# Kernel tuning notes

Hardware: AMD Instinct MI355X
Metric: run time of the kernel (lower is better)

## Reference

```python
import jax, jax.numpy as jnp
import numpy as np

N_NODES = 100000
N_EDGES = 1600000
N_CRYS = 2000
NODE_F = 64
EDGE_F = 41
N_CONV = 3
H_F = 128
EPS = 1e-5


def _seg_mean(v, idx, n):
    s = jax.ops.segment_sum(v, idx, num_segments=n)
    c = jax.ops.segment_sum(jnp.ones((v.shape[0], 1), v.dtype), idx, num_segments=n)
    return s / jnp.maximum(c, 1.0)


def _bn(x, g, b):
    # training-mode batch norm over dim 0, biased variance (torch semantics)
    m = x.mean(axis=0)
    v = x.var(axis=0)
    return (x - m) * jax.lax.rsqrt(v + EPS) * g + b


def setup_inputs() -> dict:
    key = jax.random.key(0)
    ks = jax.random.split(key, 16)
    inp = {}
    inp['node_fea'] = jax.random.randint(ks[0], (N_NODES,), 0, 101)
    inp['edge_fea'] = jax.random.normal(ks[1], (N_EDGES, EDGE_F), dtype=jnp.float32)
    inp['idx1'] = jax.random.randint(ks[2], (N_EDGES,), 0, N_NODES)
    inp['idx2'] = jax.random.randint(ks[3], (N_EDGES,), 0, N_NODES)
    inp['idx3'] = jnp.sort(jax.random.randint(ks[4], (N_NODES,), 0, N_CRYS))
    # parameters
    din = 2 * NODE_F + EDGE_F
    sc = 1.0 / np.sqrt(din)
    inp['emb'] = jax.random.normal(ks[5], (101, NODE_F), dtype=jnp.float32)
    inp['Wf'] = jax.random.uniform(ks[6], (N_CONV, din, 2 * NODE_F), jnp.float32, -sc, sc)
    inp['bf'] = jax.random.uniform(ks[7], (N_CONV, 2 * NODE_F), jnp.float32, -sc, sc)
    inp['g1'] = jnp.ones((N_CONV, 2 * NODE_F), jnp.float32)
    inp['be1'] = jnp.zeros((N_CONV, 2 * NODE_F), jnp.float32)
    inp['g2'] = jnp.ones((N_CONV, NODE_F), jnp.float32)
    inp['be2'] = jnp.zeros((N_CONV, NODE_F), jnp.float32)
    sc2 = 1.0 / np.sqrt(NODE_F)
    inp['Wc'] = jax.random.uniform(ks[8], (NODE_F, H_F), jnp.float32, -sc2, sc2)
    inp['bc'] = jax.random.uniform(ks[9], (H_F,), jnp.float32, -sc2, sc2)
    sc3 = 1.0 / np.sqrt(H_F)
    inp['Wo'] = jax.random.uniform(ks[10], (H_F, 2), jnp.float32, -sc3, sc3)
    inp['bo'] = jax.random.uniform(ks[11], (2,), jnp.float32, -sc3, sc3)
    return inp


def reference(node_fea, edge_fea, idx1, idx2, idx3, emb, Wf, bf, g1, be1, g2, be2, Wc, bc, Wo, bo):
    x = emb[node_fea]                                   # [N, 64]
    for l in range(N_CONV):
        z12 = jnp.concatenate([x[idx1], x[idx2], edge_fea], axis=1)   # [E, 169]
        z12 = _bn(z12 @ Wf[l] + bf[l], g1[l], be1[l])   # [E, 128]
        gate, conv = jnp.split(z12, 2, axis=1)
        msg = jax.nn.sigmoid(gate) * jax.nn.softplus(conv)
        node_new = _bn(_seg_mean(msg, idx1, N_NODES), g2[l], be2[l])
        x = jax.nn.softplus(x + node_new)
    crys = _seg_mean(x, idx3, N_CRYS)                   # [C, 64]
    crys = jax.nn.softplus(crys @ Wc + bc)              # [C, 128]
    return crys @ Wo + bo                               # [C, 2]
```

## Files before the change

### kernel.cpp

```cpp
#include <hip/hip_runtime.h>
#include <hip/hip_bf16.h>


#define NN 100000
#define NE 1600000
#define NC 2000
#define KPAD 176
#define NFRAG 11
#define EFW 48
#define EPSB 1e-5f
#define NCH 1000
#define CH 100

typedef _Float16 f16;
typedef _Float16 half8 __attribute__((ext_vector_type(8)));
typedef _Float16 half2v __attribute__((ext_vector_type(2)));
typedef float f32x16 __attribute__((ext_vector_type(16)));

__device__ __forceinline__ f32x16 zero16() {
    f32x16 v;
#pragma unroll
    for (int i = 0; i < 16; i++) v[i] = 0.f;
    return v;
}
__device__ __forceinline__ float fsoftplus(float x) {
    return fmaxf(x, 0.f) + __logf(1.f + __expf(-fabsf(x)));
}
__device__ __forceinline__ float fsigmoid(float x) {
    return __fdividef(1.f, 1.f + __expf(-x));
}

__global__ void k_prep_x(const int* __restrict__ nf, const float* __restrict__ emb,
                         float* __restrict__ xf, f16* __restrict__ x16) {
    for (int idx = blockIdx.x * blockDim.x + threadIdx.x; idx < NN * 64;
         idx += gridDim.x * blockDim.x) {
        int n = idx >> 6, k = idx & 63;
        float v = emb[nf[n] * 64 + k];
        xf[idx] = v;
        x16[idx] = (f16)v;
    }
}

__global__ void k_deg(const int* __restrict__ idx1, const int* __restrict__ idx3,
                      int* deg1, float* cnt3) {
    for (int i = blockIdx.x * blockDim.x + threadIdx.x; i < NE;
         i += gridDim.x * blockDim.x) {
        atomicAdd(&deg1[idx1[i]], 1);
        if (i < NN) atomicAdd(&cnt3[idx3[i]], 1.f);
    }
}

__global__ void k_scan_a(const int* __restrict__ deg, int* __restrict__ csum) {
    int t = blockIdx.x * blockDim.x + threadIdx.x;
    if (t < NCH) {
        int s = 0;
        int base = t * CH;
        for (int i = 0; i < CH; i++) s += deg[base + i];
        csum[t] = s;
    }
}
__global__ void k_scan_b(const int* __restrict__ csum, int* __restrict__ coff) {
    __shared__ int sc[256];
    int t = threadIdx.x;
    int v[4];
    int part = 0;
#pragma unroll
    for (int q = 0; q < 4; q++) {
        int idx = 4 * t + q;
        v[q] = (idx < NCH) ? csum[idx] : 0;
        part += v[q];
    }
    sc[t] = part;
    __syncthreads();
    for (int off = 1; off < 256; off <<= 1) {
        int add = (t >= off) ? sc[t - off] : 0;
        __syncthreads();
        sc[t] += add;
        __syncthreads();
    }
    int run = sc[t] - part;
#pragma unroll
    for (int q = 0; q < 4; q++) {
        int idx = 4 * t + q;
        if (idx < NCH) coff[idx] = run;
        run += v[q];
    }
}
__global__ void k_scan_c(const int* __restrict__ deg, const int* __restrict__ coff,
                         int* __restrict__ rp) {
    int t = blockIdx.x * blockDim.x + threadIdx.x;
    if (t < NCH) {
        int running = coff[t];
        int base = t * CH;
        for (int i = 0; i < CH; i++) {
            rp[base + i] = running;
            running += deg[base + i];
        }
    }
}

__global__ void k_scatter(const int* __restrict__ idx1, const int* __restrict__ idx2,
                          const int* __restrict__ rp1, int* cur1, int* elist1,
                          int* i1r, int* i2r) {
    for (int e = blockIdx.x * blockDim.x + threadIdx.x; e < NE;
         e += gridDim.x * blockDim.x) {
        int n1 = idx1[e];
        int p = rp1[n1] + atomicAdd(&cur1[n1], 1);
        elist1[p] = e;
        i1r[p] = n1;
        i2r[p] = idx2[e];
    }
}

__global__ void k_prep_efg(const float* __restrict__ ef, const int* __restrict__ elist1,
                           f16* __restrict__ ef16p) {
    for (long idx = (long)blockIdx.x * blockDim.x + threadIdx.x; idx < (long)NE * EFW;
         idx += (long)gridDim.x * blockDim.x) {
        long p = idx / EFW;
        int k = (int)(idx - p * EFW);
        int e = elist1[p];
        float v = (k < 41) ? ef[(size_t)e * 41 + k] : 0.f;
        ef16p[idx] = (f16)v;
    }
}

__global__ void k_wt(const float* __restrict__ Wf_l, f16* __restrict__ WTp) {
    for (int idx = blockIdx.x * blockDim.x + threadIdx.x; idx < 128 * KPAD;
         idx += gridDim.x * blockDim.x) {
        int sl = idx / KPAD, k = idx % KPAD;
        int g = sl >> 5, cl = sl & 31;
        int col = (cl & 16) ? 64 + g * 16 + (cl & 15) : g * 16 + cl;
        float v = (k < 169) ? Wf_l[k * 128 + col] : 0.f;
        WTp[idx] = (f16)v;
    }
}

__global__ __launch_bounds__(256) void k_edge_a(
    const f16* __restrict__ x16, const f16* __restrict__ ef16p,
    const f16* __restrict__ WTp, const int* __restrict__ i1r,
    const int* __restrict__ i2r, float* __restrict__ estats,
    f16* __restrict__ zph) {
    __shared__ f16 ldsB[NFRAG][128][16];
    __shared__ float lst[256];
    int tid = threadIdx.x;
    for (int i = tid; i < NFRAG * 128 * 2; i += 256) {
        int s = i >> 8, rem = i & 255;
        int slot = rem >> 1, half = rem & 1;
        *reinterpret_cast<half8*>(&ldsB[s][slot][half * 8]) =
            *reinterpret_cast<const half8*>(WTp + slot * KPAD + s * 16 + half * 8);
    }
    lst[tid] = 0.f;
    __syncthreads();

    int lane = tid & 63;
    int c = lane & 31, kg = lane >> 5;
    const int zbase = 2 * (c & 15) + ((c >> 4) & 1);
    const int ldso = c * 32 + kg * 16;

    float s1[4] = {0.f, 0.f, 0.f, 0.f}, s2[4] = {0.f, 0.f, 0.f, 0.f};

    const int NT = NE / 32;
    const int wstride = gridDim.x * 4;
    int t = blockIdx.x * 4 + (tid >> 6);

    half8 a[NFRAG];
    {
        size_t pb = (size_t)t * 32 + c;
        int i1v = i1r[pb], i2v = i2r[pb];
#pragma unroll
        for (int s = 0; s < 4; s++)
            a[s] = *reinterpret_cast<const half8*>(x16 + (size_t)i1v * 64 + s * 16 + kg * 8);
#pragma unroll
        for (int s = 0; s < 4; s++)
            a[4 + s] = *reinterpret_cast<const half8*>(x16 + (size_t)i2v * 64 + s * 16 + kg * 8);
#pragma unroll
        for (int s = 0; s < 3; s++)
            a[8 + s] = __builtin_nontemporal_load(
                reinterpret_cast<const half8*>(ef16p + pb * EFW + s * 16 + kg * 8));
    }
    int tn = t + wstride;
    int i1n = 0, i2n = 0;
    if (tn < NT) {
        i1n = i1r[(size_t)tn * 32 + c];
        i2n = i2r[(size_t)tn * 32 + c];
    }

    while (true) {
        bool hasn = (tn < NT);
        half8 nx[NFRAG];
        int i1nn = 0, i2nn = 0;
        if (hasn) {
#pragma unroll
            for (int s = 0; s < 4; s++)
                nx[s] = *reinterpret_cast<const half8*>(x16 + (size_t)i1n * 64 + s * 16 + kg * 8);
#pragma unroll
            for (int s = 0; s < 4; s++)
                nx[4 + s] = *reinterpret_cast<const half8*>(x16 + (size_t)i2n * 64 + s * 16 + kg * 8);
#pragma unroll
            for (int s = 0; s < 3; s++)
                nx[8 + s] = __builtin_nontemporal_load(reinterpret_cast<const half8*>(
                    ef16p + ((size_t)tn * 32 + c) * EFW + s * 16 + kg * 8));
            int tnn = tn + wstride;
            if (tnn < NT) {
                i1nn = i1r[(size_t)tnn * 32 + c];
                i2nn = i2r[(size_t)tnn * 32 + c];
            }
        }
        int p0 = t * 32;
#pragma unroll
        for (int g = 0; g < 4; g++) {
            f32x16 acc = zero16();
#pragma unroll
            for (int s = 0; s < NFRAG; s++) {
                half8 b = *reinterpret_cast<const half8*>(
                    reinterpret_cast<const char*>(&ldsB[0][0][0]) + s * 4096 + g * 1024 + ldso);
                acc = __builtin_amdgcn_mfma_f32_32x32x16_f16(a[s], b, acc, 0, 0, 0);
            }
#pragma unroll
            for (int r = 0; r < 16; r++) {
                float v = acc[r];
                s1[g] += v;
                s2[g] += v * v;
                int row = (r & 3) + 8 * (r >> 2) + 4 * kg;
                __builtin_nontemporal_store(
                    (f16)v, zph + (size_t)(p0 + row) * 128 + 32 * g + zbase);
            }
        }
        if (!hasn) break;
        t = tn;
        tn += wstride;
#pragma unroll
        for (int s = 0; s < NFRAG; s++) a[s] = nx[s];
        i1n = i1nn;
        i2n = i2nn;
    }
#pragma unroll
    for (int g = 0; g < 4; g++) {
        s1[g] += __shfl_xor(s1[g], 32, 64);
        s2[g] += __shfl_xor(s2[g], 32, 64);
    }
    if (kg == 0) {
#pragma unroll
        for (int g = 0; g < 4; g++) {
            int jz = (c & 16) ? 64 + g * 16 + (c & 15) : g * 16 + c;
            atomicAdd(&lst[jz], s1[g]);
            atomicAdd(&lst[128 + jz], s2[g]);
        }
    }
    __syncthreads();
    atomicAdd(&estats[tid], lst[tid]);
}

__global__ __launch_bounds__(256) void k_nodered(
    const half2v* __restrict__ zp, const int* __restrict__ rp1,
    const int* __restrict__ deg1, const float* __restrict__ estats,
    const float* __restrict__ g1, const float* __restrict__ be1,
    float* __restrict__ raw_out, float* __restrict__ nstats) {
    __shared__ float sstat[128];
    int tid = threadIdx.x;
    int j = tid & 63, wv = tid >> 6;
    if (tid < 128) sstat[tid] = 0.f;
    __syncthreads();
    float mg = estats[j] * (1.f / NE);
    float vg = estats[128 + j] * (1.f / NE) - mg * mg;
    float ag = g1[j] * rsqrtf(vg + EPSB);
    float bg = be1[j] - mg * ag;
    float mc = estats[64 + j] * (1.f / NE);
    float vc = estats[192 + j] * (1.f / NE) - mc * mc;
    float ac = g1[64 + j] * rsqrtf(vc + EPSB);
    float bc = be1[64 + j] - mc * ac;
    float p1 = 0.f, p2 = 0.f;
    for (int n = blockIdx.x * 4 + wv; n < NN; n += gridDim.x * 4) {
        int st = rp1[n], d = deg1[n];
        float acc = 0.f;
#pragma unroll 4
        for (int q = 0; q < d; q++) {
            half2v z = __builtin_nontemporal_load(&zp[(size_t)(st + q) * 64 + j]);
            float g = fsigmoid((float)z[0] * ag + bg);
            float s = fsoftplus((float)z[1] * ac + bc);
            acc += g * s;
        }
        float raw = acc / fmaxf((float)d, 1.f);
        raw_out[(size_t)n * 64 + j] = raw;
        p1 += raw;
        p2 += raw * raw;
    }
    atomicAdd(&sstat[j], p1);
    atomicAdd(&sstat[64 + j], p2);
    __syncthreads();
    if (tid < 128) atomicAdd(&nstats[tid], sstat[tid]);
}

template <bool LAST>
__global__ __launch_bounds__(256) void k_node_apply(
    const float* __restrict__ raw_in, const float* __restrict__ nstats,
    const float* __restrict__ g2, const float* __restrict__ be2,
    float* __restrict__ xf, f16* __restrict__ x16, const int* __restrict__ idx3,
    float* __restrict__ crsum) {
    for (int idx = blockIdx.x * blockDim.x + threadIdx.x; idx < NN * 64;
         idx += gridDim.x * blockDim.x) {
        int n = idx >> 6, j = idx & 63;
        float m = nstats[j] * (1.f / NN);
        float var = nstats[64 + j] * (1.f / NN) - m * m;
        float rs = rsqrtf(var + EPSB);
        float a = g2[j] * rs;
        float b = be2[j] - m * a;
        float v = fsoftplus(xf[idx] + raw_in[idx] * a + b);
        if (LAST) {
            atomicAdd(&crsum[(size_t)idx3[n] * 64 + j], v);
        } else {
            xf[idx] = v;
            x16[idx] = (f16)v;
        }
    }
}

__global__ __launch_bounds__(128) void k_out(const float* __restrict__ crsum,
                                             const float* __restrict__ cnt3,
                                             const float* __restrict__ Wc,
                                             const float* __restrict__ bcv,
                                             const float* __restrict__ Wo,
                                             const float* __restrict__ bo,
                                             float* __restrict__ out) {
    __shared__ float crym[64];
    __shared__ float red[4];
    int c = blockIdx.x, tid = threadIdx.x;
    if (tid < 64) crym[tid] = crsum[c * 64 + tid] / fmaxf(cnt3[c], 1.f);
    __syncthreads();
    float hv = bcv[tid];
#pragma unroll
    for (int k = 0; k < 64; k++) hv += crym[k] * Wc[k * 128 + tid];
    hv = fsoftplus(hv);
    float o0 = hv * Wo[tid * 2 + 0];
    float o1 = hv * Wo[tid * 2 + 1];
#pragma unroll
    for (int off = 32; off > 0; off >>= 1) {
        o0 += __shfl_down(o0, off, 64);
        o1 += __shfl_down(o1, off, 64);
    }
    int wv = tid >> 6;
    if ((tid & 63) == 0) { red[wv * 2] = o0; red[wv * 2 + 1] = o1; }
    __syncthreads();
    if (tid == 0) {
        out[c * 2 + 0] = red[0] + red[2] + bo[0];
        out[c * 2 + 1] = red[1] + red[3] + bo[1];
    }
}

static inline size_t al256(size_t x) { return (x + 255) & ~(size_t)255; }

extern "C" void kernel_launch(void* const* d_in, const int* in_sizes, int n_in,
                              void* d_out, int out_size, void* d_ws, size_t ws_size,
                              hipStream_t stream) {
    const int* node_fea = (const int*)d_in[0];
    const float* edge_fea = (const float*)d_in[1];
    const int* idx1 = (const int*)d_in[2];
    const int* idx2 = (const int*)d_in[3];
    const int* idx3 = (const int*)d_in[4];
    const float* emb = (const float*)d_in[5];
    const float* Wf = (const float*)d_in[6];
    const float* g1 = (const float*)d_in[8];
    const float* be1 = (const float*)d_in[9];
    const float* g2 = (const float*)d_in[10];
    const float* be2 = (const float*)d_in[11];
    const float* Wc = (const float*)d_in[12];
    const float* bc = (const float*)d_in[13];
    const float* Wo = (const float*)d_in[14];
    const float* bo = (const float*)d_in[15];
    float* out = (float*)d_out;
    unsigned char* ws = (unsigned char*)d_ws;

    size_t off = 0;
    size_t o_xf = off;     off = al256(off + (size_t)NN * 64 * 4);
    size_t o_x16 = off;    off = al256(off + (size_t)NN * 64 * 2);
    size_t o_efp = off;    off = al256(off + (size_t)NE * EFW * 2);
    size_t o_WT = off;     off = al256(off + (size_t)128 * KPAD * 2);
    size_t o_rp1 = off;    off = al256(off + (size_t)NN * 4);
    size_t o_el1 = off;    off = al256(off + (size_t)NE * 4);
    size_t o_i1r = off;    off = al256(off + (size_t)NE * 4);
    size_t o_i2r = off;    off = al256(off + (size_t)NE * 4);
    size_t o_raw = off;    off = al256(off + (size_t)NN * 64 * 4);
    size_t o_deg1 = off;   off = al256(off + (size_t)NN * 4);
    size_t o_cur1 = off;   off = al256(off + (size_t)NN * 4);
    size_t o_cnt3 = off;   off = al256(off + (size_t)NC * 4);
    size_t o_csum = off;   off = al256(off + 1024 * 4);
    size_t o_coff = off;   off = al256(off + 1024 * 4);
    size_t o_crsum = off;  off = al256(off + (size_t)NC * 64 * 4);
    size_t prep_zero_end = off;
    size_t o_estats = off; off = al256(off + 256 * 4);
    size_t o_nstats = off; off = al256(off + 128 * 4);
    size_t layer_zero_end = off;
    size_t o_z = off;      off = al256(off + (size_t)NE * 64 * 4);
    (void)ws_size;

    float* xf = (float*)(ws + o_xf);
    f16* x16 = (f16*)(ws + o_x16);
    f16* ef16p = (f16*)(ws + o_efp);
    f16* WTp = (f16*)(ws + o_WT);
    int* rp1 = (int*)(ws + o_rp1);
    int* elist1 = (int*)(ws + o_el1);
    int* i1r = (int*)(ws + o_i1r);
    int* i2r = (int*)(ws + o_i2r);
    float* raw = (float*)(ws + o_raw);
    int* deg1 = (int*)(ws + o_deg1);
    int* cur1 = (int*)(ws + o_cur1);
    float* cnt3 = (float*)(ws + o_cnt3);
    int* csum = (int*)(ws + o_csum);
    int* coff = (int*)(ws + o_coff);
    float* crsum = (float*)(ws + o_crsum);
    float* estats = (float*)(ws + o_estats);
    float* nstats = (float*)(ws + o_nstats);
    f16* zph = (f16*)(ws + o_z);
    half2v* zp = (half2v*)(ws + o_z);

    hipMemsetAsync(ws + o_deg1, 0, prep_zero_end - o_deg1, stream);
    k_prep_x<<<1024, 256, 0, stream>>>(node_fea, emb, xf, x16);
    k_deg<<<2048, 256, 0, stream>>>(idx1, idx3, deg1, cnt3);
    k_scan_a<<<4, 256, 0, stream>>>(deg1, csum);
    k_scan_b<<<1, 256, 0, stream>>>(csum, coff);
    k_scan_c<<<4, 256, 0, stream>>>(deg1, coff, rp1);
    k_scatter<<<2048, 256, 0, stream>>>(idx1, idx2, rp1, cur1, elist1, i1r, i2r);
    k_prep_efg<<<4096, 256, 0, stream>>>(edge_fea, elist1, ef16p);

    for (int l = 0; l < 3; l++) {
        const float* Wf_l = Wf + (size_t)l * 169 * 128;
        hipMemsetAsync(ws + o_estats, 0, layer_zero_end - o_estats, stream);
        k_wt<<<88, 256, 0, stream>>>(Wf_l, WTp);
        k_edge_a<<<2048, 256, 0, stream>>>(x16, ef16p, WTp, i1r, i2r, estats, zph);
        k_nodered<<<4096, 256, 0, stream>>>(zp, rp1, deg1, estats, g1 + l * 128,
                                            be1 + l * 128, raw, nstats);
        if (l < 2) {
            k_node_apply<false><<<1024, 256, 0, stream>>>(raw, nstats, g2 + l * 64,
                                                          be2 + l * 64, xf, x16,
                                                          idx3, crsum);
        } else {
            k_node_apply<true><<<1024, 256, 0, stream>>>(raw, nstats, g2 + l * 64,
                                                         be2 + l * 64, xf, x16,
                                                         idx3, crsum);
        }
    }
    k_out<<<2000, 128, 0, stream>>>(crsum, cnt3, Wc, bc, Wo, bo, out);
}
```

Before: 1.755 ms.

## Drop software prefetch in edge GEMM, use 512-thread blocks for occupancy

The edge-stage MFMA kernel no longer double-buffers gathered operands in registers. It becomes a plain grid-stride loop, runs 512-thread blocks with a launch-bounds occupancy hint, and launches half as many blocks. Nontemporal load and store hints are replaced with ordinary accesses. The intent is to free registers so more waves stay resident and hide gather latency through occupancy instead of explicit prefetch. The risk is losing the within-wave overlap and changing cache behaviour for the streamed edge features and outputs.

```diff
diff --git a/kernel.cpp b/kernel.cpp
--- a/kernel.cpp
+++ b/kernel.cpp
@@ -135,7 +135,7 @@
     }
 }
 
-__global__ __launch_bounds__(256) void k_edge_a(
+__global__ __launch_bounds__(512, 5) void k_edge_a(
     const f16* __restrict__ x16, const f16* __restrict__ ef16p,
     const f16* __restrict__ WTp, const int* __restrict__ i1r,
     const int* __restrict__ i2r, float* __restrict__ estats,
@@ -143,13 +143,13 @@
     __shared__ f16 ldsB[NFRAG][128][16];
     __shared__ float lst[256];
     int tid = threadIdx.x;
-    for (int i = tid; i < NFRAG * 128 * 2; i += 256) {
+    for (int i = tid; i < NFRAG * 128 * 2; i += 512) {
         int s = i >> 8, rem = i & 255;
         int slot = rem >> 1, half = rem & 1;
         *reinterpret_cast<half8*>(&ldsB[s][slot][half * 8]) =
             *reinterpret_cast<const half8*>(WTp + slot * KPAD + s * 16 + half * 8);
     }
-    lst[tid] = 0.f;
+    if (tid < 256) lst[tid] = 0.f;
     __syncthreads();
 
     int lane = tid & 63;
@@ -160,13 +160,11 @@
     float s1[4] = {0.f, 0.f, 0.f, 0.f}, s2[4] = {0.f, 0.f, 0.f, 0.f};
 
     const int NT = NE / 32;
-    const int wstride = gridDim.x * 4;
-    int t = blockIdx.x * 4 + (tid >> 6);
-
-    half8 a[NFRAG];
-    {
+    const int wstride = gridDim.x * 8;
+    for (int t = blockIdx.x * 8 + (tid >> 6); t < NT; t += wstride) {
         size_t pb = (size_t)t * 32 + c;
         int i1v = i1r[pb], i2v = i2r[pb];
+        half8 a[NFRAG];
 #pragma unroll
         for (int s = 0; s < 4; s++)
             a[s] = *reinterpret_cast<const half8*>(x16 + (size_t)i1v * 64 + s * 16 + kg * 8);
@@ -175,37 +173,8 @@
             a[4 + s] = *reinterpret_cast<const half8*>(x16 + (size_t)i2v * 64 + s * 16 + kg * 8);
 #pragma unroll
         for (int s = 0; s < 3; s++)
-            a[8 + s] = __builtin_nontemporal_load(
-                reinterpret_cast<const half8*>(ef16p + pb * EFW + s * 16 + kg * 8));
-    }
-    int tn = t + wstride;
-    int i1n = 0, i2n = 0;
-    if (tn < NT) {
-        i1n = i1r[(size_t)tn * 32 + c];
-        i2n = i2r[(size_t)tn * 32 + c];
-    }
-
-    while (true) {
-        bool hasn = (tn < NT);
-        half8 nx[NFRAG];
-        int i1nn = 0, i2nn = 0;
-        if (hasn) {
-#pragma unroll
-            for (int s = 0; s < 4; s++)
-                nx[s] = *reinterpret_cast<const half8*>(x16 + (size_t)i1n * 64 + s * 16 + kg * 8);
-#pragma unroll
-            for (int s = 0; s < 4; s++)
-                nx[4 + s] = *reinterpret_cast<const half8*>(x16 + (size_t)i2n * 64 + s * 16 + kg * 8);
-#pragma unroll
-            for (int s = 0; s < 3; s++)
-                nx[8 + s] = __builtin_nontemporal_load(reinterpret_cast<const half8*>(
-                    ef16p + ((size_t)tn * 32 + c) * EFW + s * 16 + kg * 8));
-            int tnn = tn + wstride;
-            if (tnn < NT) {
-                i1nn = i1r[(size_t)tnn * 32 + c];
-                i2nn = i2r[(size_t)tnn * 32 + c];
-            }
-        }
+            a[8 + s] = *reinterpret_cast<const half8*>(ef16p + pb * EFW + s * 16 + kg * 8);
+
         int p0 = t * 32;
 #pragma unroll
         for (int g = 0; g < 4; g++) {
@@ -222,17 +191,9 @@
                 s1[g] += v;
                 s2[g] += v * v;
                 int row = (r & 3) + 8 * (r >> 2) + 4 * kg;
-                __builtin_nontemporal_store(
-                    (f16)v, zph + (size_t)(p0 + row) * 128 + 32 * g + zbase);
+                zph[(size_t)(p0 + row) * 128 + 32 * g + zbase] = (f16)v;
             }
         }
-        if (!hasn) break;
-        t = tn;
-        tn += wstride;
-#pragma unroll
-        for (int s = 0; s < NFRAG; s++) a[s] = nx[s];
-        i1n = i1nn;
-        i2n = i2nn;
     }
 #pragma unroll
     for (int g = 0; g < 4; g++) {
@@ -248,7 +209,7 @@
         }
     }
     __syncthreads();
-    atomicAdd(&estats[tid], lst[tid]);
+    if (tid < 256) atomicAdd(&estats[tid], lst[tid]);
 }
 
 __global__ __launch_bounds__(256) void k_nodered(
@@ -426,7 +387,7 @@
         const float* Wf_l = Wf + (size_t)l * 169 * 128;
         hipMemsetAsync(ws + o_estats, 0, layer_zero_end - o_estats, stream);
         k_wt<<<88, 256, 0, stream>>>(Wf_l, WTp);
-        k_edge_a<<<2048, 256, 0, stream>>>(x16, ef16p, WTp, i1r, i2r, estats, zph);
+        k_edge_a<<<1024, 512, 0, stream>>>(x16, ef16p, WTp, i1r, i2r, estats, zph);
         k_nodered<<<4096, 256, 0, stream>>>(zp, rp1, deg1, estats, g1 + l * 128,
                                             be1 + l * 128, raw, nstats);
         if (l < 2) {
```

Measured after the change: 2.512 ms. 1.43x slower.
